# Kernel tuning notes

Measured on AMD Instinct MI355X. Metric: run time of the kernel, lower is better.

## Reference

```python
import jax, jax.numpy as jnp
import numpy as np

BETA = 2.0
EPS2 = 0.001 * 0.001
N_CLS = 5  # number of region classes present in mask


def setup_inputs() -> dict:
    key = jax.random.key(0)
    k1, k2, k3 = jax.random.split(key, 3)
    B, C, H, W = 16, 512, 64, 64
    feature_rec = jax.random.normal(k1, (B, C, H, W), dtype=jnp.float32)
    feature_align = jax.random.normal(k2, (B, C, H, W), dtype=jnp.float32)
    mask = jax.random.randint(k3, (B, H, W), 0, N_CLS, dtype=jnp.int32)
    return {"feature_rec": feature_rec, "feature_align": feature_align, "mask": mask}


def reference(feature_rec, feature_align, mask):
    # per-pixel mse averaged over channels -> [B, H, W]
    diff = feature_rec - feature_align
    loss_metric = jnp.mean(diff * diff, axis=1)

    # detached copy used for region reweighting (torch: clone().detach())
    w = jax.lax.stop_gradient(loss_metric)
    B, H, W = w.shape

    # segment-mean per (batch, region-class): replaces the double python loop
    seg = (mask.astype(jnp.int32) + jnp.arange(B, dtype=jnp.int32)[:, None, None] * N_CLS).reshape(-1)
    wf = w.reshape(-1)
    sums = jax.ops.segment_sum(wf, seg, num_segments=B * N_CLS)
    counts = jax.ops.segment_sum(jnp.ones_like(wf), seg, num_segments=B * N_CLS)
    avg = sums / jnp.maximum(counts, 1.0)  # empty regions untouched (never gathered)
    w = avg[seg].reshape(B, H, W)

    wmax = jnp.max(w)
    w = jnp.where(wmax > 0, w / (wmax + EPS2), w + EPS2)
    w = jnp.clip(w, 0.0, 1.0)

    return jnp.mean(loss_metric * (w * BETA + 1.0))
```

## Files before the change

### kernel.cpp

```cpp
#include <hip/hip_runtime.h>

#define Bd 16
#define Cd 512
#define Hd 64
#define Wd 64
#define HWd (Hd * Wd)
#define NCLS 5
#define BETA 2.0f
#define EPS2 (0.001f * 0.001f)

typedef float f4 __attribute__((ext_vector_type(4)));

constexpr int CH = 8;
constexpr int NCCHUNK = Cd / CH;
constexpr int PIX_PER_BLOCK = 1024;

__global__ __launch_bounds__(256, 8) void seg_partial_kernel(
    const float* __restrict__ rec, const float* __restrict__ aln,
    const int* __restrict__ mask,
    float* __restrict__ segsum, float* __restrict__ segcnt)
{
    __shared__ float binS[NCLS];
    __shared__ float binC[NCLS];
    const int tid = threadIdx.x;
    if (tid < NCLS) { binS[tid] = 0.0f; binC[tid] = 0.0f; }
    __syncthreads();

    const int b   = blockIdx.y;
    const int hw0 = blockIdx.x * PIX_PER_BLOCK + tid * 4;
    const int c0  = blockIdx.z * CH;

    const size_t base = (size_t)(b * Cd + c0) * HWd + hw0;
    const f4* __restrict__ rv = (const f4*)(rec + base);
    const f4* __restrict__ av = (const f4*)(aln + base);
    constexpr int CSTRIDE = HWd / 4;

    const int4 m = *(const int4*)(mask + b * HWd + hw0);

    float accx = 0.f, accy = 0.f, accz = 0.f, accw = 0.f;

#pragma unroll
    for (int batch = 0; batch < 2; ++batch) {
        const f4* r4 = rv + (size_t)(batch * 4) * CSTRIDE;
        const f4* a4 = av + (size_t)(batch * 4) * CSTRIDE;
        f4 R[4], A[4];
#pragma unroll
        for (int j = 0; j < 4; ++j) R[j] = __builtin_nontemporal_load(r4 + (size_t)j * CSTRIDE);
#pragma unroll
        for (int j = 0; j < 4; ++j) A[j] = __builtin_nontemporal_load(a4 + (size_t)j * CSTRIDE);
#pragma unroll
        for (int j = 0; j < 4; ++j) {
            float d;
            d = R[j].x - A[j].x; accx += d * d;
            d = R[j].y - A[j].y; accy += d * d;
            d = R[j].z - A[j].z; accz += d * d;
            d = R[j].w - A[j].w; accw += d * d;
        }
    }

    const float scale = 1.0f / (float)Cd;
    atomicAdd(&binS[m.x], accx * scale);
    atomicAdd(&binS[m.y], accy * scale);
    atomicAdd(&binS[m.z], accz * scale);
    atomicAdd(&binS[m.w], accw * scale);
    if (blockIdx.z == 0) {
        atomicAdd(&binC[m.x], 1.0f);
        atomicAdd(&binC[m.y], 1.0f);
        atomicAdd(&binC[m.z], 1.0f);
        atomicAdd(&binC[m.w], 1.0f);
    }
    __syncthreads();
    if (tid < NCLS) {
        atomicAdd(&segsum[b * NCLS + tid], binS[tid]);
        if (blockIdx.z == 0) atomicAdd(&segcnt[b * NCLS + tid], binC[tid]);
    }
}

__global__ __launch_bounds__(128) void finalize_kernel(
    const float* __restrict__ segsum, const float* __restrict__ segcnt,
    float* __restrict__ out)
{
    __shared__ float sMax[128];
    __shared__ float sSum[128];
    const int t = threadIdx.x;

    float s = 0.0f, cnt = 0.0f;
    if (t < Bd * NCLS) { s = segsum[t]; cnt = segcnt[t]; }
    const float avg = s / fmaxf(cnt, 1.0f);

    sMax[t] = avg;
    __syncthreads();
#pragma unroll
    for (int off = 64; off > 0; off >>= 1) {
        if (t < off) sMax[t] = fmaxf(sMax[t], sMax[t + off]);
        __syncthreads();
    }
    const float wmax = sMax[0];

    float w = (wmax > 0.0f) ? (avg / (wmax + EPS2)) : (avg + EPS2);
    w = fminf(fmaxf(w, 0.0f), 1.0f);

    sSum[t] = s * (w * BETA + 1.0f);
    __syncthreads();
#pragma unroll
    for (int off = 64; off > 0; off >>= 1) {
        if (t < off) sSum[t] += sSum[t + off];
        __syncthreads();
    }
    if (t == 0) out[0] = sSum[0] / (float)(Bd * HWd);
}

extern "C" void kernel_launch(void* const* d_in, const int* in_sizes, int n_in,
                              void* d_out, int out_size, void* d_ws, size_t ws_size,
                              hipStream_t stream) {
    const float* rec  = (const float*)d_in[0];
    const float* aln  = (const float*)d_in[1];
    const int*   mask = (const int*)d_in[2];
    float* out = (float*)d_out;

    float* segsum = (float*)d_ws;
    float* segcnt = segsum + Bd * NCLS;

    (void)hipMemsetAsync(d_ws, 0, 2 * Bd * NCLS * sizeof(float), stream);

    dim3 grid(HWd / PIX_PER_BLOCK, Bd, NCCHUNK);
    seg_partial_kernel<<<grid, 256, 0, stream>>>(rec, aln, mask, segsum, segcnt);
    finalize_kernel<<<1, 128, 0, stream>>>(segsum, segcnt, out);
}
```

Before: 267.9 us.

## Restructure segment reduction: blocks cover full channel planes with per-class register accumulators

```diff
diff --git a/kernel.cpp b/kernel.cpp
--- a/kernel.cpp
+++ b/kernel.cpp
@@ -11,9 +11,10 @@
 
 typedef float f4 __attribute__((ext_vector_type(4)));
 
-constexpr int CH = 8;
+constexpr int CH = 4;
 constexpr int NCCHUNK = Cd / CH;
-constexpr int PIX_PER_BLOCK = 1024;
+constexpr int F4_PER_BLOCK = CH * HWd / 4;
+constexpr int NIT = F4_PER_BLOCK / 256;
 
 __global__ __launch_bounds__(256, 8) void seg_partial_kernel(
     const float* __restrict__ rec, const float* __restrict__ aln,
@@ -22,57 +23,93 @@
 {
     __shared__ float binS[NCLS];
     __shared__ float binC[NCLS];
-    const int tid = threadIdx.x;
-    if (tid < NCLS) { binS[tid] = 0.0f; binC[tid] = 0.0f; }
+    const int t = threadIdx.x;
+    if (t < NCLS) { binS[t] = 0.0f; binC[t] = 0.0f; }
     __syncthreads();
 
-    const int b   = blockIdx.y;
-    const int hw0 = blockIdx.x * PIX_PER_BLOCK + tid * 4;
-    const int c0  = blockIdx.z * CH;
+    const int cz = blockIdx.x;
+    const int b  = blockIdx.y;
 
-    const size_t base = (size_t)(b * Cd + c0) * HWd + hw0;
-    const f4* __restrict__ rv = (const f4*)(rec + base);
-    const f4* __restrict__ av = (const f4*)(aln + base);
-    constexpr int CSTRIDE = HWd / 4;
+    const size_t base4 = ((size_t)(b * Cd + cz * CH) * HWd) / 4;
+    const f4* __restrict__ rv = (const f4*)rec + base4;
+    const f4* __restrict__ av = (const f4*)aln + base4;
+    const int4* __restrict__ mv = (const int4*)(mask + b * HWd);
 
-    const int4 m = *(const int4*)(mask + b * HWd + hw0);
+    int4 M[4];
+#pragma unroll
+    for (int j = 0; j < 4; ++j) M[j] = mv[j * 256 + t];
 
-    float accx = 0.f, accy = 0.f, accz = 0.f, accw = 0.f;
+    float acc[NCLS] = {0.f, 0.f, 0.f, 0.f, 0.f};
+    float cnt[NCLS] = {0.f, 0.f, 0.f, 0.f, 0.f};
 
 #pragma unroll
-    for (int batch = 0; batch < 2; ++batch) {
-        const f4* r4 = rv + (size_t)(batch * 4) * CSTRIDE;
-        const f4* a4 = av + (size_t)(batch * 4) * CSTRIDE;
-        f4 R[4], A[4];
+    for (int it = 0; it < NIT; it += 2) {
+        const int g0 = it * 256 + t;
+        const int g1 = (it + 1) * 256 + t;
+        f4 R0 = __builtin_nontemporal_load(rv + g0);
+        f4 A0 = __builtin_nontemporal_load(av + g0);
+        f4 R1 = __builtin_nontemporal_load(rv + g1);
+        f4 A1 = __builtin_nontemporal_load(av + g1);
+        const int4 m0 = M[it & 3];
+        const int4 m1 = M[(it + 1) & 3];
+
+        float d0x = R0.x - A0.x; d0x *= d0x;
+        float d0y = R0.y - A0.y; d0y *= d0y;
+        float d0z = R0.z - A0.z; d0z *= d0z;
+        float d0w = R0.w - A0.w; d0w *= d0w;
+        float d1x = R1.x - A1.x; d1x *= d1x;
+        float d1y = R1.y - A1.y; d1y *= d1y;
+        float d1z = R1.z - A1.z; d1z *= d1z;
+        float d1w = R1.w - A1.w; d1w *= d1w;
+
 #pragma unroll
-        for (int j = 0; j < 4; ++j) R[j] = __builtin_nontemporal_load(r4 + (size_t)j * CSTRIDE);
-#pragma unroll
-        for (int j = 0; j < 4; ++j) A[j] = __builtin_nontemporal_load(a4 + (size_t)j * CSTRIDE);
-#pragma unroll
-        for (int j = 0; j < 4; ++j) {
-            float d;
-            d = R[j].x - A[j].x; accx += d * d;
-            d = R[j].y - A[j].y; accy += d * d;
-            d = R[j].z - A[j].z; accz += d * d;
-            d = R[j].w - A[j].w; accw += d * d;
+        for (int c = 0; c < NCLS; ++c) {
+            acc[c] += ((m0.x == c) ? d0x : 0.f) + ((m0.y == c) ? d0y : 0.f)
+                    + ((m0.z == c) ? d0z : 0.f) + ((m0.w == c) ? d0w : 0.f)
+                    + ((m1.x == c) ? d1x : 0.f) + ((m1.y == c) ? d1y : 0.f)
+                    + ((m1.z == c) ? d1z : 0.f) + ((m1.w == c) ? d1w : 0.f);
         }
     }
 
-    const float scale = 1.0f / (float)Cd;
-    atomicAdd(&binS[m.x], accx * scale);
-    atomicAdd(&binS[m.y], accy * scale);
-    atomicAdd(&binS[m.z], accz * scale);
-    atomicAdd(&binS[m.w], accw * scale);
-    if (blockIdx.z == 0) {
-        atomicAdd(&binC[m.x], 1.0f);
-        atomicAdd(&binC[m.y], 1.0f);
-        atomicAdd(&binC[m.z], 1.0f);
-        atomicAdd(&binC[m.w], 1.0f);
+    if (cz == 0) {
+#pragma unroll
+        for (int j = 0; j < 4; ++j) {
+#pragma unroll
+            for (int c = 0; c < NCLS; ++c) {
+                cnt[c] += (float)((M[j].x == c) + (M[j].y == c)
+                                + (M[j].z == c) + (M[j].w == c));
+            }
+        }
+    }
+
+#pragma unroll
+    for (int c = 0; c < NCLS; ++c) {
+#pragma unroll
+        for (int off = 32; off > 0; off >>= 1)
+            acc[c] += __shfl_xor(acc[c], off);
+    }
+    if (cz == 0) {
+#pragma unroll
+        for (int c = 0; c < NCLS; ++c) {
+#pragma unroll
+            for (int off = 32; off > 0; off >>= 1)
+                cnt[c] += __shfl_xor(cnt[c], off);
+        }
+    }
+
+    const int lane = t & 63;
+    if (lane == 0) {
+        const float scale = 1.0f / (float)Cd;
+#pragma unroll
+        for (int c = 0; c < NCLS; ++c) {
+            atomicAdd(&binS[c], acc[c] * scale);
+            if (cz == 0) atomicAdd(&binC[c], cnt[c]);
+        }
     }
     __syncthreads();
-    if (tid < NCLS) {
-        atomicAdd(&segsum[b * NCLS + tid], binS[tid]);
-        if (blockIdx.z == 0) atomicAdd(&segcnt[b * NCLS + tid], binC[tid]);
+    if (t < NCLS) {
+        atomicAdd(&segsum[b * NCLS + t], binS[t]);
+        if (cz == 0) atomicAdd(&segcnt[b * NCLS + t], binC[t]);
     }
 }
 
@@ -123,7 +160,7 @@
 
     (void)hipMemsetAsync(d_ws, 0, 2 * Bd * NCLS * sizeof(float), stream);
 
-    dim3 grid(HWd / PIX_PER_BLOCK, Bd, NCCHUNK);
+    dim3 grid(NCCHUNK, Bd);
     seg_partial_kernel<<<grid, 256, 0, stream>>>(rec, aln, mask, segsum, segcnt);
     finalize_kernel<<<1, 128, 0, stream>>>(segsum, segcnt, out);
 }
```

Measured after the change: 336.4 us. 25.6% more time.
